# Kernel optimization log

Hardware: AMD Instinct MI355X
Metric: run time of the kernel (lower is better)

The kernel has to match this reference:

```python
import jax, jax.numpy as jnp
import numpy as np


def setup_inputs() -> dict:
    key = jax.random.key(0)
    ks = jax.random.split(key, 6)
    B, S, D = 32, 4096, 512
    return {
        "inputs": jax.random.normal(ks[0], (B, S, D), dtype=jnp.float32),
        "W_y": jax.random.normal(ks[1], (D, D), dtype=jnp.float32) * 0.05,
        "W_h": jax.random.normal(ks[2], (D, D), dtype=jnp.float32) * 0.05,
        "W_p": jax.random.normal(ks[3], (D, D), dtype=jnp.float32) * 0.05,
        "W_x": jax.random.normal(ks[4], (D, D), dtype=jnp.float32) * 0.05,
        "w": jax.random.normal(ks[5], (D, 1), dtype=jnp.float32) * 0.05,
    }


def reference(inputs, W_y, W_h, W_p, W_x, w):
    # inputs: [B, S, D]; the TF einsums 'ijk,kk->ijk' etc. use only diag(W).
    half = inputs.shape[1] // 2
    y = inputs[:, :half, :]          # [B, S/2, D] premise states
    h_n = inputs[:, -1, :]           # [B, D] final hidden state
    first = y * jnp.diagonal(W_y)                     # [B, S/2, D]
    second = (h_n * jnp.diagonal(W_h))[:, None, :]    # [B, 1, D] (RepeatVector via broadcast)
    M = jnp.tanh(first + second)                      # [B, S/2, D]
    scores = jnp.einsum('bsd,d->bs', M, w[:, 0])      # [B, S/2]
    alpha = jax.nn.softmax(scores, axis=-1)           # softmax over attended positions
    r = jnp.einsum('bsd,bs->bd', y, alpha)            # [B, D] weighted sum
    return jnp.tanh(r * jnp.diagonal(W_p) + h_n * jnp.diagonal(W_x))
```

## Files before the change

### kernel.cpp

```cpp
#include <hip/hip_runtime.h>

#define DDIM 512
#define HALF 2048
#define BATCH 32
#define S_TOTAL 4096
#define NCHUNK 64
#define ROWS_PER_CHUNK (HALF / NCHUNK)
#define LOG2E 1.44269504088896340736f
#define SHIFT2 32.0f

__device__ __forceinline__ float fast_tanh(float x) {
    float e = __builtin_amdgcn_exp2f(x * 2.88539008177792681472f);
    return 1.0f - 2.0f * __builtin_amdgcn_rcpf(e + 1.0f);
}

__device__ __forceinline__ float tanh_poly(float x) {
    const float c3 = -0.33333333333f, c5 = 0.13333333333f,
                c7 = -0.05396825397f, c9 = 0.02186948854f;
    float x2 = x * x;
    float p = fmaf(x2, c9, c7);
    p = fmaf(x2, p, c5);
    p = fmaf(x2, p, c3);
    return fmaf(x * x2, p, x);
}

__global__ __launch_bounds__(256) void pass1_kernel(
    const float* __restrict__ inputs, const float* __restrict__ Wy,
    const float* __restrict__ Wh, const float* __restrict__ wvec,
    float* __restrict__ ws_l, float* __restrict__ ws_r)
{
    const int chunk = blockIdx.x;
    const int b = blockIdx.y;
    const int tid = threadIdx.x;
    const int wave = tid >> 6;
    const int lane = tid & 63;
    const int d0 = lane * 8;

    float wy[8], wv[8], c[8];
    {
        const float* hn_row = inputs + ((size_t)b * S_TOTAL + (S_TOTAL - 1)) * DDIM;
#pragma unroll
        for (int j = 0; j < 8; ++j) {
            const int d = d0 + j;
            wy[j] = Wy[(size_t)d * (DDIM + 1)];
            wv[j] = wvec[d];
            c[j]  = hn_row[d] * Wh[(size_t)d * (DDIM + 1)];
        }
    }

    float l = 0.0f;
    float r[8];
#pragma unroll
    for (int j = 0; j < 8; ++j) r[j] = 0.0f;

    const float* base =
        inputs + ((size_t)b * S_TOTAL + (size_t)chunk * ROWS_PER_CHUNK) * DDIM + d0;

#pragma unroll
    for (int it = 0; it < ROWS_PER_CHUNK / 8; ++it) {
        const int srow = it * 8 + wave * 2;
        const float* ra = base + (size_t)srow * DDIM;
        const float* rb = ra + DDIM;
        const float4 a0 = *(const float4*)ra;
        const float4 a1 = *(const float4*)(ra + 4);
        const float4 b0 = *(const float4*)rb;
        const float4 b1 = *(const float4*)(rb + 4);
        float ya[8] = {a0.x, a0.y, a0.z, a0.w, a1.x, a1.y, a1.z, a1.w};
        float yb[8] = {b0.x, b0.y, b0.z, b0.w, b1.x, b1.y, b1.z, b1.w};

        float pa = 0.0f, pb = 0.0f;
#pragma unroll
        for (int j = 0; j < 8; ++j) {
            pa += tanh_poly(fmaf(ya[j], wy[j], c[j])) * wv[j];
            pb += tanh_poly(fmaf(yb[j], wy[j], c[j])) * wv[j];
        }
#pragma unroll
        for (int off = 1; off < 64; off <<= 1) {
            pa += __shfl_xor(pa, off);
            pb += __shfl_xor(pb, off);
        }
        const float ea = __builtin_amdgcn_exp2f(fmaf(pa, LOG2E, -SHIFT2));
        const float eb = __builtin_amdgcn_exp2f(fmaf(pb, LOG2E, -SHIFT2));
        l += ea + eb;
#pragma unroll
        for (int j = 0; j < 8; ++j) {
            r[j] = fmaf(ea, ya[j], r[j]);
            r[j] = fmaf(eb, yb[j], r[j]);
        }
    }

    __shared__ float lds_r[4][DDIM];
    __shared__ float lds_l[4];
#pragma unroll
    for (int j = 0; j < 8; ++j) lds_r[wave][d0 + j] = r[j];
    if (lane == 0) lds_l[wave] = l;
    __syncthreads();

    const size_t blk = (size_t)b * NCHUNK + chunk;
#pragma unroll
    for (int d = tid; d < DDIM; d += 256)
        ws_r[blk * DDIM + d] =
            lds_r[0][d] + lds_r[1][d] + lds_r[2][d] + lds_r[3][d];
    if (tid == 0)
        ws_l[blk] = lds_l[0] + lds_l[1] + lds_l[2] + lds_l[3];
}

__global__ __launch_bounds__(256) void pass2_kernel(
    const float* __restrict__ inputs, const float* __restrict__ Wp,
    const float* __restrict__ Wx, const float* __restrict__ ws_l,
    const float* __restrict__ ws_r, float* __restrict__ out)
{
    const int b = blockIdx.y;
    const int d = blockIdx.x * 256 + threadIdx.x;

    float L = 0.0f;
#pragma unroll 8
    for (int cidx = 0; cidx < NCHUNK; ++cidx)
        L += ws_l[b * NCHUNK + cidx];

    float acc = 0.0f;
#pragma unroll 8
    for (int cidx = 0; cidx < NCHUNK; ++cidx)
        acc += ws_r[((size_t)b * NCHUNK + cidx) * DDIM + d];

    const float r = acc * __builtin_amdgcn_rcpf(L) *
                    (L * __builtin_amdgcn_rcpf(L) > 0.0f ? 1.0f : 1.0f);
    const float hn = inputs[((size_t)b * S_TOTAL + (S_TOTAL - 1)) * DDIM + d];
    const float wp = Wp[(size_t)d * (DDIM + 1)];
    const float wx = Wx[(size_t)d * (DDIM + 1)];
    out[(size_t)b * DDIM + d] = fast_tanh(fmaf(r, wp, hn * wx));
}

extern "C" void kernel_launch(void* const* d_in, const int* in_sizes, int n_in,
                              void* d_out, int out_size, void* d_ws, size_t ws_size,
                              hipStream_t stream)
{
    const float* inputs = (const float*)d_in[0];
    const float* Wy     = (const float*)d_in[1];
    const float* Wh     = (const float*)d_in[2];
    const float* Wp     = (const float*)d_in[3];
    const float* Wx     = (const float*)d_in[4];
    const float* wvec   = (const float*)d_in[5];

    float* ws_l = (float*)d_ws;
    float* ws_r = ws_l + (size_t)BATCH * NCHUNK;

    dim3 grid1(NCHUNK, BATCH);
    pass1_kernel<<<grid1, 256, 0, stream>>>(inputs, Wy, Wh, wvec, ws_l, ws_r);

    dim3 grid2(DDIM / 256, BATCH);
    pass2_kernel<<<grid2, 256, 0, stream>>>(inputs, Wp, Wx, ws_l, ws_r,
                                            (float*)d_out);
}
```

Before: 345.0 us.

## Load all chunk rows upfront and use DPP wave reductions in pass1

Each wave now loads its 8 rows into registers in one burst, computes all 8 dot products, and then reduces them with DPP/swizzle-based wave reductions instead of shfl_xor loops. The goal is more memory-level parallelism and cheaper cross-lane reductions. The redundant expression in pass2 is also simplified. ROWS_PER_CHUNK is hardcoded to 32, the same value HALF/NCHUNK already gave, so coverage is unchanged. Holding 64 row values per thread raises register pressure.

New measurement: 350.9 us. No clear change (+1.7%).

```diff
diff --git a/kernel.cpp b/kernel.cpp
--- a/kernel.cpp
+++ b/kernel.cpp
@@ -5,7 +5,7 @@
 #define BATCH 32
 #define S_TOTAL 4096
 #define NCHUNK 64
-#define ROWS_PER_CHUNK (HALF / NCHUNK)
+#define ROWS_PER_CHUNK 32
 #define LOG2E 1.44269504088896340736f
 #define SHIFT2 32.0f
 
@@ -22,6 +22,22 @@
     p = fmaf(x2, p, c5);
     p = fmaf(x2, p, c3);
     return fmaf(x * x2, p, x);
+}
+
+template <int CTRL>
+__device__ __forceinline__ float dpp_add(float x) {
+    int yi = __builtin_amdgcn_update_dpp(0, __float_as_int(x), CTRL, 0xf, 0xf, true);
+    return x + __int_as_float(yi);
+}
+
+__device__ __forceinline__ float wave_reduce_sum(float p) {
+    p = dpp_add<0xB1>(p);
+    p = dpp_add<0x4E>(p);
+    p = dpp_add<0x141>(p);
+    p = dpp_add<0x140>(p);
+    p += __int_as_float(__builtin_amdgcn_ds_swizzle(__float_as_int(p), 0x401F));
+    p += __shfl_xor(p, 32);
+    return p;
 }
 
 __global__ __launch_bounds__(256) void pass1_kernel(
@@ -48,45 +64,43 @@
         }
     }
 
+    const float* rb0 = inputs +
+        ((size_t)b * S_TOTAL + (size_t)chunk * ROWS_PER_CHUNK + wave * 8) * DDIM + d0;
+    float y[8][8];
+#pragma unroll
+    for (int k = 0; k < 8; ++k) {
+        const float4 u0 = *(const float4*)(rb0 + (size_t)k * DDIM);
+        const float4 u1 = *(const float4*)(rb0 + (size_t)k * DDIM + 4);
+        y[k][0] = u0.x; y[k][1] = u0.y; y[k][2] = u0.z; y[k][3] = u0.w;
+        y[k][4] = u1.x; y[k][5] = u1.y; y[k][6] = u1.z; y[k][7] = u1.w;
+    }
+
+    float pd[8];
+#pragma unroll
+    for (int k = 0; k < 8; ++k) {
+        float p = 0.0f;
+#pragma unroll
+        for (int j = 0; j < 8; ++j)
+            p += tanh_poly(fmaf(y[k][j], wy[j], c[j])) * wv[j];
+        pd[k] = p;
+    }
+#pragma unroll
+    for (int k = 0; k < 8; ++k) pd[k] = wave_reduce_sum(pd[k]);
+
+    float e[8];
     float l = 0.0f;
+#pragma unroll
+    for (int k = 0; k < 8; ++k) {
+        e[k] = __builtin_amdgcn_exp2f(fmaf(pd[k], LOG2E, -SHIFT2));
+        l += e[k];
+    }
     float r[8];
 #pragma unroll
-    for (int j = 0; j < 8; ++j) r[j] = 0.0f;
-
-    const float* base =
-        inputs + ((size_t)b * S_TOTAL + (size_t)chunk * ROWS_PER_CHUNK) * DDIM + d0;
-
+    for (int j = 0; j < 8; ++j) {
+        float acc = e[0] * y[0][j];
 #pragma unroll
-    for (int it = 0; it < ROWS_PER_CHUNK / 8; ++it) {
-        const int srow = it * 8 + wave * 2;
-        const float* ra = base + (size_t)srow * DDIM;
-        const float* rb = ra + DDIM;
-        const float4 a0 = *(const float4*)ra;
-        const float4 a1 = *(const float4*)(ra + 4);
-        const float4 b0 = *(const float4*)rb;
-        const float4 b1 = *(const float4*)(rb + 4);
-        float ya[8] = {a0.x, a0.y, a0.z, a0.w, a1.x, a1.y, a1.z, a1.w};
-        float yb[8] = {b0.x, b0.y, b0.z, b0.w, b1.x, b1.y, b1.z, b1.w};
-
-        float pa = 0.0f, pb = 0.0f;
-#pragma unroll
-        for (int j = 0; j < 8; ++j) {
-            pa += tanh_poly(fmaf(ya[j], wy[j], c[j])) * wv[j];
-            pb += tanh_poly(fmaf(yb[j], wy[j], c[j])) * wv[j];
-        }
-#pragma unroll
-        for (int off = 1; off < 64; off <<= 1) {
-            pa += __shfl_xor(pa, off);
-            pb += __shfl_xor(pb, off);
-        }
-        const float ea = __builtin_amdgcn_exp2f(fmaf(pa, LOG2E, -SHIFT2));
-        const float eb = __builtin_amdgcn_exp2f(fmaf(pb, LOG2E, -SHIFT2));
-        l += ea + eb;
-#pragma unroll
-        for (int j = 0; j < 8; ++j) {
-            r[j] = fmaf(ea, ya[j], r[j]);
-            r[j] = fmaf(eb, yb[j], r[j]);
-        }
+        for (int k = 1; k < 8; ++k) acc = fmaf(e[k], y[k][j], acc);
+        r[j] = acc;
     }
 
     __shared__ float lds_r[4][DDIM];
@@ -123,8 +137,7 @@
     for (int cidx = 0; cidx < NCHUNK; ++cidx)
         acc += ws_r[((size_t)b * NCHUNK + cidx) * DDIM + d];
 
-    const float r = acc * __builtin_amdgcn_rcpf(L) *
-                    (L * __builtin_amdgcn_rcpf(L) > 0.0f ? 1.0f : 1.0f);
+    const float r = acc * __builtin_amdgcn_rcpf(L);
     const float hn = inputs[((size_t)b * S_TOTAL + (S_TOTAL - 1)) * DDIM + d];
     const float wp = Wp[(size_t)d * (DDIM + 1)];
     const float wx = Wx[(size_t)d * (DDIM + 1)];
```
